# Kernel optimization log

Hardware: AMD Instinct MI355X
Metric: run time of the kernel (lower is better)

The kernel has to match this reference:

```python
import jax, jax.numpy as jnp
import numpy as np

D = 768          # wav2vec2-base hidden size
H = 4            # cross-attn heads
HD = D // H
B = 8
N = 1024         # w2v sequence length (target length)
T = 2000         # raw CQCC frames
N_GAT = 3
NUM_CLASSES = 2


def _p(key, shape, scale=0.02):
    return jax.random.normal(key, shape, dtype=jnp.float32) * scale


def layer_norm(x, g, b, eps=1e-5):
    m = x.mean(-1, keepdims=True)
    v = x.var(-1, keepdims=True)
    return (x - m) * jax.lax.rsqrt(v + eps) * g + b


def gelu(x):
    return jax.nn.gelu(x, approximate=False)


def conv1d(x, w, b):
    # x [B,C,T], w [O,I,K], padding=1 (same)
    y = jax.lax.conv_general_dilated(x, w, (1,), [(1, 1)], dimension_numbers=('NCH', 'OIH', 'NCH'))
    return y + b[None, :, None]


def batchnorm(x, g, b, m, v, eps=1e-5):
    # eval-mode BatchNorm1d on [B,C,T]
    return (x - m[None, :, None]) * jax.lax.rsqrt(v[None, :, None] + eps) * g[None, :, None] + b[None, :, None]


def interp_linear(x, target_len):
    # torch F.interpolate(mode='linear', align_corners=False); x [B,T,D] -> [B,target_len,D]
    t_in = x.shape[1]
    pos = (jnp.arange(target_len, dtype=jnp.float32) + 0.5) * (t_in / target_len) - 0.5
    pos = jnp.clip(pos, 0.0, t_in - 1.0)
    lo = jnp.floor(pos).astype(jnp.int32)
    hi = jnp.minimum(lo + 1, t_in - 1)
    w = (pos - lo.astype(jnp.float32))[None, :, None]
    return x[:, lo] * (1.0 - w) + x[:, hi] * w


def mha(q, k, v, in_w, in_b, out_w, out_b):
    # torch nn.MultiheadAttention, batch_first=True
    bb, nq, _ = q.shape
    nk = k.shape[1]
    wq, wk, wv = in_w[:D], in_w[D:2 * D], in_w[2 * D:]
    bq, bk, bv = in_b[:D], in_b[D:2 * D], in_b[2 * D:]
    qh = (q @ wq.T + bq).reshape(bb, nq, H, HD).transpose(0, 2, 1, 3)
    kh = (k @ wk.T + bk).reshape(bb, nk, H, HD).transpose(0, 2, 1, 3)
    vh = (v @ wv.T + bv).reshape(bb, nk, H, HD).transpose(0, 2, 1, 3)
    scores = jnp.einsum('bhqd,bhkd->bhqk', qh, kh) * (1.0 / np.sqrt(HD))
    alpha = jax.nn.softmax(scores, axis=-1)
    o = jnp.einsum('bhqk,bhkd->bhqd', alpha, vh).transpose(0, 2, 1, 3).reshape(bb, nq, D)
    return o @ out_w.T + out_b


def graph_attn(x, fc_w, fc_b, a_w, a_b):
    # GAT score on concat([h_i, h_j]) decomposes additively: e_ij = a_i.h_i + a_j.h_j + b
    h = x @ fc_w.T + fc_b                      # [B,N,D]
    s_i = h @ a_w[:D]                          # [B,N]
    s_j = h @ a_w[D:]                          # [B,N]
    e = s_i[:, :, None] + s_j[:, None, :] + a_b  # [B,N,N]
    alpha = jax.nn.softmax(e, axis=-1)
    return jnp.einsum('bij,bjd->bid', alpha, h)


def _forward(w2v, cqcc, conv1_w, conv1_b, bn1_g, bn1_b, bn1_m, bn1_v,
             conv2_w, conv2_b, bn2_g, bn2_b, bn2_m, bn2_v, pos_embed,
             lnq_g, lnq_b, lnkv_g, lnkv_b,
             a1_in_w, a1_in_b, a1_out_w, a1_out_b,
             a2_in_w, a2_in_b, a2_out_w, a2_out_b,
             gat_fc_w, gat_fc_b, gat_a_w, gat_a_b, gln_g, gln_b,
             clf_w1, clf_b1, clf_w2, clf_b2):
    # CQCC conv stack
    x = gelu(batchnorm(conv1d(cqcc, conv1_w, conv1_b), bn1_g, bn1_b, bn1_m, bn1_v))
    x = gelu(batchnorm(conv1d(x, conv2_w, conv2_b), bn2_g, bn2_b, bn2_m, bn2_v))  # [B,D,T]
    cq = interp_linear(x.transpose(0, 2, 1), w2v.shape[1])  # [B,N,D]
    # shared positional encoding
    n = w2v.shape[1]
    w = w2v + pos_embed[:, :n]
    cq = cq + pos_embed[:, :n]
    # bidirectional cross attention (norm_q / norm_kv shared across directions)
    out1 = mha(layer_norm(cq, lnq_g, lnq_b), layer_norm(w, lnkv_g, lnkv_b),
               layer_norm(w, lnkv_g, lnkv_b), a1_in_w, a1_in_b, a1_out_w, a1_out_b)
    out2 = mha(layer_norm(w, lnq_g, lnq_b), layer_norm(cq, lnkv_g, lnkv_b),
               layer_norm(cq, lnkv_g, lnkv_b), a2_in_w, a2_in_b, a2_out_w, a2_out_b)
    x = out1 + out2
    # 3 residual graph-attention blocks
    for l in range(N_GAT):
        res = x
        x = graph_attn(x, gat_fc_w[l], gat_fc_b[l], gat_a_w[l], gat_a_b[l])
        x = layer_norm(x + res, gln_g[l], gln_b[l])
    pooled = x.mean(axis=1)
    h = gelu(pooled @ clf_w1.T + clf_b1)
    return h @ clf_w2.T + clf_b2


def setup_inputs():
    ks = iter(jax.random.split(jax.random.key(0), 64))
    inp = {}
    inp['w2v'] = jax.random.normal(next(ks), (B, N, D), dtype=jnp.float32)
    inp['cqcc'] = jax.random.normal(next(ks), (B, 20, T), dtype=jnp.float32)
    inp['conv1_w'] = _p(next(ks), (128, 20, 3)); inp['conv1_b'] = jnp.zeros((128,), jnp.float32)
    inp['bn1_g'] = jnp.ones((128,), jnp.float32); inp['bn1_b'] = jnp.zeros((128,), jnp.float32)
    inp['bn1_m'] = jnp.zeros((128,), jnp.float32); inp['bn1_v'] = jnp.ones((128,), jnp.float32)
    inp['conv2_w'] = _p(next(ks), (D, 128, 3)); inp['conv2_b'] = jnp.zeros((D,), jnp.float32)
    inp['bn2_g'] = jnp.ones((D,), jnp.float32); inp['bn2_b'] = jnp.zeros((D,), jnp.float32)
    inp['bn2_m'] = jnp.zeros((D,), jnp.float32); inp['bn2_v'] = jnp.ones((D,), jnp.float32)
    inp['pos_embed'] = _p(next(ks), (1, 2000, D), 1.0)
    inp['lnq_g'] = jnp.ones((D,), jnp.float32); inp['lnq_b'] = jnp.zeros((D,), jnp.float32)
    inp['lnkv_g'] = jnp.ones((D,), jnp.float32); inp['lnkv_b'] = jnp.zeros((D,), jnp.float32)
    inp['a1_in_w'] = _p(next(ks), (3 * D, D)); inp['a1_in_b'] = jnp.zeros((3 * D,), jnp.float32)
    inp['a1_out_w'] = _p(next(ks), (D, D)); inp['a1_out_b'] = jnp.zeros((D,), jnp.float32)
    inp['a2_in_w'] = _p(next(ks), (3 * D, D)); inp['a2_in_b'] = jnp.zeros((3 * D,), jnp.float32)
    inp['a2_out_w'] = _p(next(ks), (D, D)); inp['a2_out_b'] = jnp.zeros((D,), jnp.float32)
    inp['gat_fc_w'] = _p(next(ks), (N_GAT, D, D)); inp['gat_fc_b'] = jnp.zeros((N_GAT, D), jnp.float32)
    inp['gat_a_w'] = _p(next(ks), (N_GAT, 2 * D)); inp['gat_a_b'] = jnp.zeros((N_GAT,), jnp.float32)
    inp['gln_g'] = jnp.ones((N_GAT, D), jnp.float32); inp['gln_b'] = jnp.zeros((N_GAT, D), jnp.float32)
    inp['clf_w1'] = _p(next(ks), (128, D)); inp['clf_b1'] = jnp.zeros((128,), jnp.float32)
    inp['clf_w2'] = _p(next(ks), (NUM_CLASSES, 128)); inp['clf_b2'] = jnp.zeros((NUM_CLASSES,), jnp.float32)
    return inp


def reference(w2v, cqcc, conv1_w, conv1_b, bn1_g, bn1_b, bn1_m, bn1_v,
              conv2_w, conv2_b, bn2_g, bn2_b, bn2_m, bn2_v, pos_embed,
              lnq_g, lnq_b, lnkv_g, lnkv_b,
              a1_in_w, a1_in_b, a1_out_w, a1_out_b,
              a2_in_w, a2_in_b, a2_out_w, a2_out_b,
              gat_fc_w, gat_fc_b, gat_a_w, gat_a_b, gln_g, gln_b,
              clf_w1, clf_b1, clf_w2, clf_b2):
    return _forward(w2v, cqcc, conv1_w, conv1_b, bn1_g, bn1_b, bn1_m, bn1_v,
                    conv2_w, conv2_b, bn2_g, bn2_b, bn2_m, bn2_v, pos_embed,
                    lnq_g, lnq_b, lnkv_g, lnkv_b,
                    a1_in_w, a1_in_b, a1_out_w, a1_out_b,
                    a2_in_w, a2_in_b, a2_out_w, a2_out_b,
                    gat_fc_w, gat_fc_b, gat_a_w, gat_a_b, gln_g, gln_b,
                    clf_w1, clf_b1, clf_w2, clf_b2)
```

## Files before the change

### kernel.cpp

```cpp
#include <hip/hip_runtime.h>
#include <math.h>

#define DD 768
#define NH 4
#define HDIM 192
#define BBATCH 8
#define NSEQ 1024
#define TLEN 2000
#define SLOT 6291456

typedef _Float16 h16;
typedef _Float16 half8v __attribute__((ext_vector_type(8)));
typedef _Float16 half4v __attribute__((ext_vector_type(4)));
typedef float f32x4 __attribute__((ext_vector_type(4)));

__device__ __forceinline__ float gelu_f(float x){
  return 0.5f * x * (1.0f + erff(x * 0.70710678118654752440f));
}
__device__ __forceinline__ float wave_sum(float v){
  #pragma unroll
  for (int off = 32; off; off >>= 1) v += __shfl_xor(v, off);
  return v;
}
__device__ __forceinline__ float wave_max(float v){
  #pragma unroll
  for (int off = 32; off; off >>= 1) v = fmaxf(v, __shfl_xor(v, off));
  return v;
}
__device__ __forceinline__ void gload16(const h16* g, h16* l){
  __builtin_amdgcn_global_load_lds(
      (const __attribute__((address_space(1))) void*)g,
      (__attribute__((address_space(3))) void*)l, 16, 0, 0);
}
__device__ __forceinline__ int xcd_remap(int orig, int nwg){
  int q = nwg >> 3, r = nwg & 7;
  int xcd = orig & 7, idx = orig >> 3;
  return (xcd < r ? xcd * (q + 1) : r * (q + 1) + (xcd - r) * q) + idx;
}

__global__ __launch_bounds__(256) void k_cast(const float* __restrict__ s,
    h16* __restrict__ d, int n){
  int i = blockIdx.x * 256 + threadIdx.x;
  if (i < n) d[i] = (h16)s[i];
}

__global__ __launch_bounds__(256) void k_conv1t(const float* __restrict__ cqcc,
    const float* __restrict__ w, const float* __restrict__ bias,
    const float* __restrict__ g, const float* __restrict__ be,
    const float* __restrict__ mm, const float* __restrict__ vv,
    float* __restrict__ out){
  __shared__ float xs[20][258];
  __shared__ float wsm[32*60];
  const int t0 = blockIdx.x * 256;
  const int ocg = blockIdx.y, b = blockIdx.z;
  const int tid = threadIdx.x;
  for (int idx = tid; idx < 20*258; idx += 256){
    int ic = idx / 258, tt = idx % 258;
    int t = t0 + tt - 1;
    xs[ic][tt] = (t >= 0 && t < TLEN) ? cqcc[((size_t)b*20 + ic)*TLEN + t] : 0.f;
  }
  for (int idx = tid; idx < 32*60; idx += 256)
    wsm[idx] = w[ocg*32*60 + idx];
  __syncthreads();
  int t = t0 + tid;
  if (t >= TLEN) return;
  float acc[32] = {};
  for (int ic = 0; ic < 20; ++ic){
    float x0 = xs[ic][tid], x1v = xs[ic][tid+1], x2v = xs[ic][tid+2];
    #pragma unroll
    for (int oc = 0; oc < 32; ++oc){
      const float* wp = &wsm[(oc*20 + ic)*3];
      acc[oc] += wp[0]*x0 + wp[1]*x1v + wp[2]*x2v;
    }
  }
  #pragma unroll 4
  for (int oc = 0; oc < 32; ++oc){
    int c = ocg*32 + oc;
    float s = rsqrtf(vv[c] + 1e-5f) * g[c];
    float val = (acc[oc] + bias[c] - mm[c]) * s + be[c];
    out[((size_t)b*128 + c)*TLEN + t] = gelu_f(val);
  }
}

__global__ __launch_bounds__(256) void k_im2col(const float* __restrict__ x1,
    h16* __restrict__ A2){
  int idx = blockIdx.x * 256 + threadIdx.x;
  if (idx >= 16000*384) return;
  int c = idx % 384, m = idx / 384;
  int b = m / TLEN, t = m % TLEN;
  int ic = c / 3, kh = c % 3;
  int ts = t + kh - 1;
  float v = (ts < 0 || ts >= TLEN) ? 0.f : x1[((size_t)b*128 + ic)*TLEN + ts];
  A2[idx] = (h16)v;
}

__global__ void k_bnprep(const float* __restrict__ cb, const float* __restrict__ g,
    const float* __restrict__ be, const float* __restrict__ m,
    const float* __restrict__ v, float* __restrict__ sc, float* __restrict__ off){
  int i = blockIdx.x * 256 + threadIdx.x;
  if (i >= DD) return;
  float s = g[i] * rsqrtf(v[i] + 1e-5f);
  sc[i] = s;
  off[i] = (cb[i] - m[i]) * s + be[i];
}

__global__ __launch_bounds__(256) void k_interp_ln(const h16* __restrict__ x2,
    const float* __restrict__ pe,
    const float* __restrict__ g1, const float* __restrict__ b1, h16* __restrict__ o1,
    const float* __restrict__ g2, const float* __restrict__ b2, h16* __restrict__ o2){
  __shared__ float ss[4], sqq[4];
  int row = blockIdx.x, tid = threadIdx.x;
  int b = row >> 10, i = row & 1023;
  float p = (i + 0.5f) * ((float)TLEN / (float)NSEQ) - 0.5f;
  p = fminf(fmaxf(p, 0.f), (float)(TLEN - 1));
  int lo = (int)floorf(p);
  int hi = min(lo + 1, TLEN - 1);
  float w = p - (float)lo;
  const h16* blo = x2 + ((size_t)b * TLEN + lo) * DD;
  const h16* bhi = x2 + ((size_t)b * TLEN + hi) * DD;
  const float* per = pe + (size_t)i * DD;
  float v[3]; float s = 0.f, sq = 0.f;
  #pragma unroll
  for (int j = 0; j < 3; ++j){
    int d = j * 256 + tid;
    float x = (float)blo[d] * (1.f - w) + (float)bhi[d] * w + per[d];
    v[j] = x; s += x; sq += x * x;
  }
  s = wave_sum(s); sq = wave_sum(sq);
  int wv = tid >> 6;
  if ((tid & 63) == 0){ ss[wv] = s; sqq[wv] = sq; }
  __syncthreads();
  s  = ss[0] + ss[1] + ss[2] + ss[3];
  sq = sqq[0] + sqq[1] + sqq[2] + sqq[3];
  float mean = s * (1.f / DD);
  float var  = sq * (1.f / DD) - mean * mean;
  float r = rsqrtf(var + 1e-5f);
  #pragma unroll
  for (int j = 0; j < 3; ++j){
    int d = j * 256 + tid;
    float xn = (v[j] - mean) * r;
    o1[(size_t)row * DD + d] = (h16)(xn * g1[d] + b1[d]);
    o2[(size_t)row * DD + d] = (h16)(xn * g2[d] + b2[d]);
  }
}

__global__ __launch_bounds__(256) void k_addpos_ln(const float* __restrict__ xin,
    const float* __restrict__ pe,
    const float* __restrict__ g1, const float* __restrict__ b1, h16* __restrict__ o1,
    const float* __restrict__ g2, const float* __restrict__ b2, h16* __restrict__ o2){
  __shared__ float ss[4], sqq[4];
  int row = blockIdx.x, tid = threadIdx.x;
  int i = row & 1023;
  const float* ip = xin + (size_t)row * DD;
  const float* per = pe + (size_t)i * DD;
  float v[3]; float s = 0.f, sq = 0.f;
  #pragma unroll
  for (int j = 0; j < 3; ++j){
    int d = j * 256 + tid;
    float x = ip[d] + per[d];
    v[j] = x; s += x; sq += x * x;
  }
  s = wave_sum(s); sq = wave_sum(sq);
  int wv = tid >> 6;
  if ((tid & 63) == 0){ ss[wv] = s; sqq[wv] = sq; }
  __syncthreads();
  s  = ss[0] + ss[1] + ss[2] + ss[3];
  sq = sqq[0] + sqq[1] + sqq[2] + sqq[3];
  float mean = s * (1.f / DD);
  float var  = sq * (1.f / DD) - mean * mean;
  float r = rsqrtf(var + 1e-5f);
  #pragma unroll
  for (int j = 0; j < 3; ++j){
    int d = j * 256 + tid;
    float xn = (v[j] - mean) * r;
    o1[(size_t)row * DD + d] = (h16)(xn * g1[d] + b1[d]);
    o2[(size_t)row * DD + d] = (h16)(xn * g2[d] + b2[d]);
  }
}

__global__ __launch_bounds__(256) void k_lnH(const h16* __restrict__ in,
    const float* __restrict__ ctx, const float* __restrict__ g,
    const float* __restrict__ be, h16* __restrict__ out){
  __shared__ float ss[4], sqq[4];
  int row = blockIdx.x, tid = threadIdx.x;
  const h16* ip = in + (size_t)row * DD;
  int b = row >> 10;
  float v[3]; float s = 0.f, sq = 0.f;
  #pragma unroll
  for (int j = 0; j < 3; ++j){
    int d = j * 256 + tid;
    float x = (float)ip[d] + ctx[b * DD + d];
    v[j] = x; s += x; sq += x * x;
  }
  s = wave_sum(s); sq = wave_sum(sq);
  int w = tid >> 6;
  if ((tid & 63) == 0){ ss[w] = s; sqq[w] = sq; }
  __syncthreads();
  s  = ss[0] + ss[1] + ss[2] + ss[3];
  sq = sqq[0] + sqq[1] + sqq[2] + sqq[3];
  float mean = s * (1.f / DD);
  float var  = sq * (1.f / DD) - mean * mean;
  float r = rsqrtf(var + 1e-5f);
  #pragma unroll
  for (int j = 0; j < 3; ++j){
    int d = j * 256 + tid;
    out[(size_t)row * DD + d] = (h16)((v[j] - mean) * r * g[d] + be[d]);
  }
}

#define GEMM_MAINLOOP(Abase, lda, Wbase, ldw, Kdim)                          \
  auto stage = [&](int buf, int kt){                                         \
    _Pragma("unroll")                                                        \
    for (int i = 0; i < 4; ++i){                                             \
      int p = i*256 + tid; int row = p >> 3; int ch = (p & 7) ^ (row & 7);   \
      gload16(Abase + (size_t)(m0+row)*lda + kt + ch*8, &Als[buf][p*8]);     \
    }                                                                        \
    _Pragma("unroll")                                                        \
    for (int i = 0; i < 4; ++i){                                             \
      int p = i*256 + tid; int row = p >> 3; int ch = (p & 7) ^ (row & 7);   \
      gload16(Wbase + (size_t)(n0+row)*ldw + kt + ch*8, &Bls[buf][p*8]);     \
    }                                                                        \
  };                                                                         \
  stage(0, 0);                                                               \
  const int nk = Kdim >> 6;                                                  \
  for (int t = 0; t < nk; ++t){                                              \
    const int cur = t & 1;                                                   \
    if (t + 1 < nk){                                                         \
      stage(cur ^ 1, (t + 1) << 6);                                          \
      asm volatile("s_waitcnt vmcnt(8)" ::: "memory");                       \
    } else {                                                                 \
      asm volatile("s_waitcnt vmcnt(0)" ::: "memory");                       \
    }                                                                        \
    __builtin_amdgcn_s_barrier();                                            \
    __builtin_amdgcn_sched_barrier(0);                                       \
    __builtin_amdgcn_s_setprio(1);                                           \
    _Pragma("unroll")                                                        \
    for (int kk = 0; kk < 2; ++kk){                                          \
      half8v af[4], bf[4];                                                   \
      _Pragma("unroll")                                                      \
      for (int mi = 0; mi < 4; ++mi){                                        \
        int row = wr*64 + mi*16 + lr;                                        \
        int chp = (kk*4 + lg) ^ (row & 7);                                   \
        af[mi] = *(const half8v*)&Als[cur][row*64 + chp*8];                  \
      }                                                                      \
      _Pragma("unroll")                                                      \
      for (int ni = 0; ni < 4; ++ni){                                        \
        int row = wc*64 + ni*16 + lr;                                        \
        int chp = (kk*4 + lg) ^ (row & 7);                                   \
        bf[ni] = *(const half8v*)&Bls[cur][row*64 + chp*8];                  \
      }                                                                      \
      _Pragma("unroll")                                                      \
      for (int mi = 0; mi < 4; ++mi)                                         \
        _Pragma("unroll")                                                    \
        for (int ni = 0; ni < 4; ++ni)                                       \
          acc[mi][ni] = __builtin_amdgcn_mfma_f32_16x16x32_f16(              \
              af[mi], bf[ni], acc[mi][ni], 0, 0, 0);                         \
    }                                                                        \
    __builtin_amdgcn_s_setprio(0);                                           \
    asm volatile("s_waitcnt lgkmcnt(0)" ::: "memory");                       \
    __builtin_amdgcn_sched_barrier(0);                                       \
    __builtin_amdgcn_s_barrier();                                            \
  }

__global__ __launch_bounds__(256) void k_gemm_h(
    const h16* __restrict__ A, const h16* __restrict__ W,
    int lda, int ldw, int ldc, int K,
    const float* __restrict__ bias, const float* __restrict__ sc,
    const float* __restrict__ off, const h16* __restrict__ addh,
    float* __restrict__ outf, h16* __restrict__ outh,
    const float* __restrict__ rdw, float* __restrict__ rdpart)
{
  __shared__ h16 Als[2][128*64];
  __shared__ h16 Bls[2][128*64];
  const int tid = threadIdx.x;
  const int gx = gridDim.x, gy = gridDim.y;
  const int wg = xcd_remap(blockIdx.x + gx * blockIdx.y, gx * gy);
  const int nidx = wg % gx;
  const int n0 = nidx * 128, m0 = (wg / gx) * 128;
  const int lane = tid & 63, wid = tid >> 6;
  const int wr = wid >> 1, wc = wid & 1;
  const int lr = lane & 15, lg = lane >> 4;
  f32x4 acc[4][4] = {};
  GEMM_MAINLOOP(A, lda, W, ldw, K)
  float rd[4][4] = {};
  #pragma unroll
  for (int mi = 0; mi < 4; ++mi){
    #pragma unroll
    for (int ni = 0; ni < 4; ++ni){
      int col = n0 + wc*64 + ni*16 + lr;
      int rowb = m0 + wr*64 + mi*16 + lg*4;
      float cb = bias ? bias[col] : 0.f;
      float aw = rdw ? rdw[col] : 0.f;
      #pragma unroll
      for (int r = 0; r < 4; ++r){
        size_t idx = (size_t)(rowb + r) * ldc + col;
        float v = acc[mi][ni][r];
        if (sc){ v = v * sc[col] + off[col]; v = gelu_f(v); }
        else v += cb;
        if (addh) v += (float)addh[idx];
        if (outf) outf[idx] = v;
        if (outh) outh[idx] = (h16)v;
        if (rdw) rd[mi][r] += v * aw;
      }
    }
  }
  if (rdw){
    #pragma unroll
    for (int mi = 0; mi < 4; ++mi){
      #pragma unroll
      for (int r = 0; r < 4; ++r){
        float p = rd[mi][r];
        #pragma unroll
        for (int o = 1; o < 16; o <<= 1) p += __shfl_xor(p, o);
        if (lr == 0){
          int row = m0 + wr*64 + mi*16 + lg*4 + r;
          rdpart[(size_t)row * 12 + nidx*2 + wc] = p;
        }
      }
    }
  }
}

__global__ __launch_bounds__(256) void k_gemm6(
    const h16* __restrict__ Lall, const h16* __restrict__ w6,
    const float* __restrict__ b1, const float* __restrict__ b2,
    h16* __restrict__ qkv6)
{
  __shared__ h16 Als[2][128*64];
  __shared__ h16 Bls[2][128*64];
  const int tid = threadIdx.x;
  const int gx = gridDim.x, gy = gridDim.y;
  const int nwg = gx * gy * 6;
  const int wg = xcd_remap(blockIdx.x + gx*(blockIdx.y + gy*blockIdx.z), nwg);
  const int n0 = (wg % gx) * 128;
  const int m0 = ((wg / gx) % gy) * 128;
  const int bz = wg / (gx * gy);
  const int aidx = (1468 >> (2*bz)) & 3;
  const h16* A = Lall + (size_t)aidx * SLOT;
  const h16* W = w6 + (size_t)bz * 589824;
  const float* bias = (bz < 3 ? b1 + bz*DD : b2 + (bz-3)*DD);
  h16* C = qkv6 + (size_t)bz * SLOT;
  const int lane = tid & 63, wid = tid >> 6;
  const int wr = wid >> 1, wc = wid & 1;
  const int lr = lane & 15, lg = lane >> 4;
  f32x4 acc[4][4] = {};
  GEMM_MAINLOOP(A, DD, W, DD, DD)
  #pragma unroll
  for (int mi = 0; mi < 4; ++mi){
    #pragma unroll
    for (int ni = 0; ni < 4; ++ni){
      int col = n0 + wc*64 + ni*16 + lr;
      int rowb = m0 + wr*64 + mi*16 + lg*4;
      float cb = bias[col];
      #pragma unroll
      for (int r = 0; r < 4; ++r)
        C[(size_t)(rowb + r) * DD + col] = (h16)(acc[mi][ni][r] + cb);
    }
  }
}

__global__ __launch_bounds__(256) void k_trV(const h16* __restrict__ Vh, int ldv,
    h16* __restrict__ VT){
  __shared__ h16 tile[64*64];
  const int z = blockIdx.z, b = z >> 2, h = z & 3;
  const int q0 = blockIdx.x * 64, d0 = blockIdx.y * 64;
  const int t = threadIdx.x;
  {
    int qq = t >> 2, ds = (t & 3) * 16;
    const h16* src = Vh + ((size_t)b*NSEQ + q0 + qq)*ldv + h*HDIM + d0 + ds;
    half8v v0 = *(const half8v*)src;
    half8v v1 = *(const half8v*)(src + 8);
    int c0 = (ds >> 3) ^ (qq & 7), c1 = ((ds >> 3) + 1) ^ (qq & 7);
    *(half8v*)&tile[qq*64 + c0*8] = v0;
    *(half8v*)&tile[qq*64 + c1*8] = v1;
  }
  __syncthreads();
  {
    int dd = t >> 2, qs = (t & 3) * 16;
    half8v o0, o1;
    #pragma unroll
    for (int j = 0; j < 8; ++j){
      int q = qs + j, q2 = qs + 8 + j;
      o0[j] = tile[q*64  + (((dd>>3) ^ (q&7))*8)  + (dd & 7)];
      o1[j] = tile[q2*64 + (((dd>>3) ^ (q2&7))*8) + (dd & 7)];
    }
    h16* dst = VT + (size_t)z*HDIM*NSEQ + (size_t)(d0+dd)*NSEQ + q0 + qs;
    *(half8v*)dst = o0;
    *(half8v*)(dst + 8) = o1;
  }
}

__global__ __launch_bounds__(256) void k_flash(const h16* __restrict__ Qp,
    const h16* __restrict__ Kp, const h16* __restrict__ VTp,
    h16* __restrict__ Op){
  __shared__ h16 Ks[2][32*192];
  __shared__ h16 Vs[2][192*32];
  __shared__ h16 Ps[4][16*32];
  const int tid = threadIdx.x;
  const int bh = blockIdx.x, qt = blockIdx.y;
  const int b = bh >> 2, h = bh & 3;
  const int q0 = qt * 64;
  const h16* Qg = Qp + (size_t)b*NSEQ*DD + h*HDIM;
  const h16* Kg = Kp + (size_t)b*NSEQ*DD + h*HDIM;
  const h16* Vg = VTp + (size_t)bh*HDIM*NSEQ;
  const int lane = tid & 63, wid = tid >> 6;
  const int lr = lane & 15, lg = lane >> 4;
  half8v qf[6];
  {
    int qrow = q0 + wid*16 + lr;
    #pragma unroll
    for (int ks = 0; ks < 6; ++ks)
      qf[ks] = *(const half8v*)(Qg + (size_t)qrow*DD + ks*32 + lg*8);
  }
  auto stageK = [&](int buf, int k0){
    #pragma unroll
    for (int i = 0; i < 3; ++i){
      int p = i*256 + tid;
      int row = p / 24, chp = p % 24;
      int ch = chp ^ (row & 7);
      gload16(Kg + (size_t)(k0+row)*DD + ch*8, &Ks[buf][p*8]);
    }
  };
  auto stageV = [&](int buf, int k0){
    #pragma unroll
    for (int i = 0; i < 3; ++i){
      int p = i*256 + tid;
      int row = p >> 2, chp = p & 3;
      int ch = chp ^ ((row >> 1) & 3);
      gload16(Vg + (size_t)row*NSEQ + k0 + ch*8, &Vs[buf][p*8]);
    }
  };
  stageK(0, 0); stageV(0, 0);
  f32x4 oacc[12] = {};
  float m_run[4] = {-1e30f, -1e30f, -1e30f, -1e30f};
  float l_run[4] = {};
  const float SC = 0.07216878364870322f;
  __syncthreads();
  for (int kt = 0; kt < 32; ++kt){
    const int cur = kt & 1;
    if (kt + 1 < 32){ stageK(cur^1, (kt+1)*32); stageV(cur^1, (kt+1)*32); }
    f32x4 sacc[2] = {};
    __builtin_amdgcn_s_setprio(1);
    #pragma unroll
    for (int ks = 0; ks < 6; ++ks){
      #pragma unroll
      for (int t = 0; t < 2; ++t){
        int krow = t*16 + lr;
        int ch = (ks*4 + lg) ^ (krow & 7);
        half8v kf = *(const half8v*)&Ks[cur][krow*192 + ch*8];
        sacc[t] = __builtin_amdgcn_mfma_f32_16x16x32_f16(qf[ks], kf, sacc[t], 0, 0, 0);
      }
    }
    __builtin_amdgcn_s_setprio(0);
    float mnew[4], c[4], psum[4];
    #pragma unroll
    for (int r = 0; r < 4; ++r){
      float mt = fmaxf(sacc[0][r], sacc[1][r]);
      #pragma unroll
      for (int off = 1; off < 16; off <<= 1) mt = fmaxf(mt, __shfl_xor(mt, off));
      mnew[r] = fmaxf(m_run[r], mt * SC);
      c[r] = __expf(m_run[r] - mnew[r]);
      psum[r] = 0.f;
    }
    #pragma unroll
    for (int t = 0; t < 2; ++t){
      #pragma unroll
      for (int r = 0; r < 4; ++r){
        float p = __expf(sacc[t][r] * SC - mnew[r]);
        psum[r] += p;
        int q = lg*4 + r, key = t*16 + lr;
        int ch = (t*2 + (lr>>3)) ^ ((q>>1) & 3);
        Ps[wid][q*32 + ch*8 + (key & 7)] = (h16)p;
      }
    }
    #pragma unroll
    for (int r = 0; r < 4; ++r){
      #pragma unroll
      for (int off = 1; off < 16; off <<= 1) psum[r] += __shfl_xor(psum[r], off);
      l_run[r] = l_run[r] * c[r] + psum[r];
      m_run[r] = mnew[r];
    }
    #pragma unroll
    for (int dt = 0; dt < 12; ++dt){
      f32x4 o = oacc[dt];
      o[0] *= c[0]; o[1] *= c[1]; o[2] *= c[2]; o[3] *= c[3];
      oacc[dt] = o;
    }
    asm volatile("s_waitcnt lgkmcnt(0)" ::: "memory");
    __builtin_amdgcn_sched_barrier(0);
    {
      int pch = lg ^ ((lr >> 1) & 3);
      half8v pf = *(const half8v*)&Ps[wid][lr*32 + pch*8];
      __builtin_amdgcn_s_setprio(1);
      #pragma unroll
      for (int dt = 0; dt < 12; ++dt){
        int drow = dt*16 + lr;
        int vch = lg ^ ((drow >> 1) & 3);
        half8v vf = *(const half8v*)&Vs[cur][drow*32 + vch*8];
        oacc[dt] = __builtin_amdgcn_mfma_f32_16x16x32_f16(pf, vf, oacc[dt], 0, 0, 0);
      }
      __builtin_amdgcn_s_setprio(0);
    }
    __syncthreads();
  }
  float inv[4];
  #pragma unroll
  for (int r = 0; r < 4; ++r) inv[r] = 1.0f / l_run[r];
  h16* Og = Op + (size_t)b*NSEQ*DD + h*HDIM;
  #pragma unroll
  for (int dt = 0; dt < 12; ++dt){
    #pragma unroll
    for (int r = 0; r < 4; ++r){
      int q = q0 + wid*16 + lg*4 + r;
      Og[(size_t)q*DD + dt*16 + lr] = (h16)(oacc[dt][r] * inv[r]);
    }
  }
}

__global__ __launch_bounds__(256) void k_softmax12(const float* __restrict__ part,
    float* __restrict__ y){
  __shared__ float red[4];
  int b = blockIdx.x, tid = threadIdx.x;
  float v[4]; float mx = -1e30f;
  #pragma unroll
  for (int j = 0; j < 4; ++j){
    int i = j * 256 + tid;
    const float* p = part + (size_t)(b * NSEQ + i) * 12;
    float s = 0.f;
    #pragma unroll
    for (int k = 0; k < 12; ++k) s += p[k];
    v[j] = s; mx = fmaxf(mx, s);
  }
  mx = wave_max(mx);
  if ((tid & 63) == 0) red[tid >> 6] = mx;
  __syncthreads();
  mx = fmaxf(fmaxf(red[0], red[1]), fmaxf(red[2], red[3]));
  __syncthreads();
  float s = 0.f;
  #pragma unroll
  for (int j = 0; j < 4; ++j){ v[j] = __expf(v[j] - mx); s += v[j]; }
  s = wave_sum(s);
  if ((tid & 63) == 0) red[tid >> 6] = s;
  __syncthreads();
  s = red[0] + red[1] + red[2] + red[3];
  float inv = 1.0f / s;
  #pragma unroll
  for (int j = 0; j < 4; ++j) y[b * NSEQ + j * 256 + tid] = v[j] * inv;
}

__global__ __launch_bounds__(256) void k_ctx1(const float* __restrict__ alpha,
    const h16* __restrict__ h, float* __restrict__ part){
  int d = blockIdx.x * 256 + threadIdx.x;
  int b = blockIdx.y, pc = blockIdx.z;
  if (d >= DD) return;
  float acc = 0.f;
  const h16* hp = h + ((size_t)b * NSEQ + pc * 64) * DD + d;
  const float* ap = alpha + b * NSEQ + pc * 64;
  #pragma unroll 4
  for (int j = 0; j < 64; ++j) acc += ap[j] * (float)hp[(size_t)j * DD];
  part[(size_t)(b * 16 + pc) * DD + d] = acc;
}
__global__ __launch_bounds__(256) void k_ctx2(const float* __restrict__ part,
    float scale, float* __restrict__ ctx){
  int d = blockIdx.x * 256 + threadIdx.x;
  int b = blockIdx.y;
  if (d >= DD) return;
  float acc = 0.f;
  #pragma unroll
  for (int p = 0; p < 16; ++p) acc += part[(size_t)(b * 16 + p) * DD + d];
  ctx[b * DD + d] = acc * scale;
}

__global__ __launch_bounds__(256) void k_pool1(const h16* __restrict__ x,
    float* __restrict__ part){
  int d = blockIdx.x * 256 + threadIdx.x;
  int b = blockIdx.y, pc = blockIdx.z;
  if (d >= DD) return;
  float acc = 0.f;
  const h16* xp = x + ((size_t)b * NSEQ + pc * 64) * DD + d;
  #pragma unroll 4
  for (int j = 0; j < 64; ++j) acc += (float)xp[(size_t)j * DD];
  part[(size_t)(b * 16 + pc) * DD + d] = acc;
}

__global__ __launch_bounds__(128) void k_clf(const float* __restrict__ pooled,
    const float* __restrict__ w1, const float* __restrict__ b1,
    const float* __restrict__ w2, const float* __restrict__ b2,
    float* __restrict__ out){
  __shared__ float pl[DD];
  __shared__ float h1[128];
  int b = blockIdx.x, tid = threadIdx.x;
  #pragma unroll
  for (int j = 0; j < 6; ++j) pl[j * 128 + tid] = pooled[b * DD + j * 128 + tid];
  __syncthreads();
  float acc = b1[tid];
  const float* wp = w1 + (size_t)tid * DD;
  for (int d = 0; d < DD; ++d) acc += pl[d] * wp[d];
  h1[tid] = gelu_f(acc);
  __syncthreads();
  if (tid < 2){
    float o = b2[tid];
    const float* w2p = w2 + tid * 128;
    for (int c = 0; c < 128; ++c) o += h1[c] * w2p[c];
    out[b * 2 + tid] = o;
  }
}

extern "C" void kernel_launch(void* const* d_in, const int* in_sizes, int n_in,
                              void* d_out, int out_size, void* d_ws, size_t ws_size,
                              hipStream_t stream){
  (void)in_sizes; (void)n_in; (void)out_size;
  const float* w2v      = (const float*)d_in[0];
  const float* cqcc     = (const float*)d_in[1];
  const float* conv1_w  = (const float*)d_in[2];
  const float* conv1_b  = (const float*)d_in[3];
  const float* bn1_g    = (const float*)d_in[4];
  const float* bn1_b    = (const float*)d_in[5];
  const float* bn1_m    = (const float*)d_in[6];
  const float* bn1_v    = (const float*)d_in[7];
  const float* conv2_w  = (const float*)d_in[8];
  const float* conv2_b  = (const float*)d_in[9];
  const float* bn2_g    = (const float*)d_in[10];
  const float* bn2_b    = (const float*)d_in[11];
  const float* bn2_m    = (const float*)d_in[12];
  const float* bn2_v    = (const float*)d_in[13];
  const float* pos_embed= (const float*)d_in[14];
  const float* lnq_g    = (const float*)d_in[15];
  const float* lnq_b    = (const float*)d_in[16];
  const float* lnkv_g   = (const float*)d_in[17];
  const float* lnkv_b   = (const float*)d_in[18];
  const float* a1_in_w  = (const float*)d_in[19];
  const float* a1_in_b  = (const float*)d_in[20];
  const float* a1_out_w = (const float*)d_in[21];
  const float* a1_out_b = (const float*)d_in[22];
  const float* a2_in_w  = (const float*)d_in[23];
  const float* a2_in_b  = (const float*)d_in[24];
  const float* a2_out_w = (const float*)d_in[25];
  const float* a2_out_b = (const float*)d_in[26];
  const float* gat_fc_w = (const float*)d_in[27];
  const float* gat_fc_b = (const float*)d_in[28];
  const float* gat_a_w  = (const float*)d_in[29];
  const float* gln_g    = (const float*)d_in[31];
  const float* gln_b    = (const float*)d_in[32];
  const float* clf_w1   = (const float*)d_in[33];
  const float* clf_b1   = (const float*)d_in[34];
  const float* clf_w2   = (const float*)d_in[35];
  const float* clf_b2   = (const float*)d_in[36];

  char* wsp = (char*)d_ws;
  auto F = [&](size_t bytes){ char* p = wsp; wsp += (bytes + 255) & ~(size_t)255; return p; };
  h16* xh      = (h16*)F(12582912);
  h16* Lall    = (h16*)F(4*12582912);
  h16* qkv6    = (h16*)F(6*12582912);
  h16* VT      = (h16*)F(12582912);
  h16* o1h     = (h16*)F(12582912);
  h16* w6      = (h16*)F(2*3538944);
  h16* w_a1out = (h16*)F(1179648);
  h16* w_a2out = (h16*)F(1179648);
  h16* w_gat   = (h16*)F(3538944);
  h16* w_c2    = (h16*)F(589824);
  float* scb   = (float*)F(3072);
  float* offb  = (float*)F(3072);
  float* alpha = (float*)F(32768);
  float* ctxb  = (float*)F(24576);
  float* pooled= (float*)F(24576);
  float* partb = (float*)F(393216);
  if ((size_t)(wsp - (char*)d_ws) > ws_size) return;

  float* x1  = (float*)Lall;
  h16*   A2  = Lall + 2*SLOT;
  h16*   x2h = qkv6;
  h16*   hh  = qkv6;

  const int NR = BBATCH * NSEQ;

  k_cast<<<(1769472+255)/256, 256, 0, stream>>>(a1_in_w,  w6,           1769472);
  k_cast<<<(1769472+255)/256, 256, 0, stream>>>(a2_in_w,  w6 + 1769472, 1769472);
  k_cast<<<(589824+255)/256,  256, 0, stream>>>(a1_out_w, w_a1out, 589824);
  k_cast<<<(589824+255)/256,  256, 0, stream>>>(a2_out_w, w_a2out, 589824);
  k_cast<<<(1769472+255)/256, 256, 0, stream>>>(gat_fc_w, w_gat,   1769472);
  k_cast<<<(294912+255)/256,  256, 0, stream>>>(conv2_w,  w_c2,    294912);
  k_bnprep<<<3, 256, 0, stream>>>(conv2_b, bn2_g, bn2_b, bn2_m, bn2_v, scb, offb);

  k_conv1t<<<dim3(8, 4, BBATCH), 256, 0, stream>>>(cqcc, conv1_w, conv1_b,
      bn1_g, bn1_b, bn1_m, bn1_v, x1);
  k_im2col<<<(16000*384+255)/256, 256, 0, stream>>>(x1, A2);
  k_gemm_h<<<dim3(6, 125), 256, 0, stream>>>(A2, w_c2, 384, 384, DD, 384,
      nullptr, scb, offb, nullptr, nullptr, x2h, nullptr, nullptr);

  k_interp_ln<<<NR, 256, 0, stream>>>(x2h, pos_embed,
      lnq_g, lnq_b, Lall, lnkv_g, lnkv_b, Lall + SLOT);
  k_addpos_ln<<<NR, 256, 0, stream>>>(w2v, pos_embed,
      lnq_g, lnq_b, Lall + 2*SLOT, lnkv_g, lnkv_b, Lall + 3*SLOT);

  k_gemm6<<<dim3(6, 64, 6), 256, 0, stream>>>(Lall, w6, a1_in_b, a2_in_b, qkv6);

  dim3 gflash(32, 16);

  k_trV<<<dim3(16, 3, 32), 256, 0, stream>>>(qkv6 + 2*(size_t)SLOT, DD, VT);
  k_flash<<<gflash, 256, 0, stream>>>(qkv6, qkv6 + (size_t)SLOT, VT, qkv6);
  k_gemm_h<<<dim3(6, 64), 256, 0, stream>>>(qkv6, w_a1out, DD, DD, DD, DD,
      a1_out_b, nullptr, nullptr, nullptr, nullptr, o1h, nullptr, nullptr);

  k_trV<<<dim3(16, 3, 32), 256, 0, stream>>>(qkv6 + 5*(size_t)SLOT, DD, VT);
  k_flash<<<gflash, 256, 0, stream>>>(qkv6 + 3*(size_t)SLOT, qkv6 + 4*(size_t)SLOT,
                                      VT, qkv6 + 3*(size_t)SLOT);
  k_gemm_h<<<dim3(6, 64), 256, 0, stream>>>(qkv6 + 3*(size_t)SLOT, w_a2out,
      DD, DD, DD, DD, a2_out_b, nullptr, nullptr, o1h, nullptr, xh, nullptr, nullptr);

  for (int l = 0; l < 3; ++l){
    k_gemm_h<<<dim3(6, 64), 256, 0, stream>>>(xh, w_gat + (size_t)l*589824,
        DD, DD, DD, DD, gat_fc_b + l*DD, nullptr, nullptr, nullptr,
        nullptr, hh, gat_a_w + l*2*DD + DD, partb);
    k_softmax12<<<BBATCH, 256, 0, stream>>>(partb, alpha);
    k_ctx1<<<dim3(3, BBATCH, 16), 256, 0, stream>>>(alpha, hh, partb);
    k_ctx2<<<dim3(3, BBATCH), 256, 0, stream>>>(partb, 1.0f, ctxb);
    k_lnH<<<NR, 256, 0, stream>>>(xh, ctxb, gln_g + l*DD, gln_b + l*DD, xh);
  }

  k_pool1<<<dim3(3, BBATCH, 16), 256, 0, stream>>>(xh, partb);
  k_ctx2<<<dim3(3, BBATCH), 256, 0, stream>>>(partb, 1.0f/NSEQ, pooled);
  k_clf<<<BBATCH, 128, 0, stream>>>(pooled, clf_w1, clf_b1, clf_w2, clf_b2,
                                    (float*)d_out);
}
```

Measured before the change: 623.0 us.

## Fuse im2col into conv2 GEMM via padded time-major fp16 layout and merge weight casts

conv1 now writes fp16 output in a zero-padded [B, T+2, 128] time-major layout. A new implicit-GEMM conv2 kernel reads the three shifted taps directly through a reordered weight matrix (kh-major), which removes the fp32 intermediate and the separate im2col pass. Five weight-cast launches are merged into one segmented kernel to cut launch overhead. The GEMM pads M to 2048 rows per batch, so some rows are computed and then discarded, and conv1's writes are now strided 64-byte chunks per thread.

```diff
diff --git a/kernel.cpp b/kernel.cpp
--- a/kernel.cpp
+++ b/kernel.cpp
@@ -8,6 +8,7 @@
 #define NSEQ 1024
 #define TLEN 2000
 #define SLOT 6291456
+#define XROW 256256
 
 typedef _Float16 h16;
 typedef _Float16 half8v __attribute__((ext_vector_type(8)));
@@ -38,17 +39,35 @@
   return (xcd < r ? xcd * (q + 1) : r * (q + 1) + (xcd - r) * q) + idx;
 }
 
-__global__ __launch_bounds__(256) void k_cast(const float* __restrict__ s,
-    h16* __restrict__ d, int n){
+struct CastArgs {
+  const float* s[5];
+  h16* d[5];
+  int cum[6];
+};
+__global__ __launch_bounds__(256) void k_cast5(CastArgs a, int total){
   int i = blockIdx.x * 256 + threadIdx.x;
-  if (i < n) d[i] = (h16)s[i];
+  if (i >= total) return;
+  int seg = 0;
+  #pragma unroll
+  for (int t = 1; t < 5; ++t) seg += (i >= a.cum[t]);
+  int off = i - a.cum[seg];
+  a.d[seg][off] = (h16)a.s[seg][off];
+}
+
+__global__ __launch_bounds__(256) void k_castc2(const float* __restrict__ s,
+    h16* __restrict__ d){
+  int i = blockIdx.x * 256 + threadIdx.x;
+  if (i >= 294912) return;
+  int oc = i / 384, rem = i % 384;
+  int ic = rem / 3, kh = rem % 3;
+  d[oc * 384 + kh * 128 + ic] = (h16)s[i];
 }
 
 __global__ __launch_bounds__(256) void k_conv1t(const float* __restrict__ cqcc,
     const float* __restrict__ w, const float* __restrict__ bias,
     const float* __restrict__ g, const float* __restrict__ be,
     const float* __restrict__ mm, const float* __restrict__ vv,
-    float* __restrict__ out){
+    h16* __restrict__ X){
   __shared__ float xs[20][258];
   __shared__ float wsm[32*60];
   const int t0 = blockIdx.x * 256;
@@ -73,25 +92,24 @@
       acc[oc] += wp[0]*x0 + wp[1]*x1v + wp[2]*x2v;
     }
   }
+  h16* dst = X + (size_t)b*XROW + (size_t)(t+1)*128 + ocg*32;
   #pragma unroll 4
   for (int oc = 0; oc < 32; ++oc){
     int c = ocg*32 + oc;
     float s = rsqrtf(vv[c] + 1e-5f) * g[c];
     float val = (acc[oc] + bias[c] - mm[c]) * s + be[c];
-    out[((size_t)b*128 + c)*TLEN + t] = gelu_f(val);
-  }
-}
-
-__global__ __launch_bounds__(256) void k_im2col(const float* __restrict__ x1,
-    h16* __restrict__ A2){
-  int idx = blockIdx.x * 256 + threadIdx.x;
-  if (idx >= 16000*384) return;
-  int c = idx % 384, m = idx / 384;
-  int b = m / TLEN, t = m % TLEN;
-  int ic = c / 3, kh = c % 3;
-  int ts = t + kh - 1;
-  float v = (ts < 0 || ts >= TLEN) ? 0.f : x1[((size_t)b*128 + ic)*TLEN + ts];
-  A2[idx] = (h16)v;
+    dst[oc] = (h16)gelu_f(val);
+  }
+  if (t == 0){
+    h16* z = X + (size_t)b*XROW + ocg*32;
+    #pragma unroll
+    for (int oc = 0; oc < 32; ++oc) z[oc] = (h16)0.f;
+  }
+  if (t == TLEN-1){
+    h16* z = X + (size_t)b*XROW + (size_t)2001*128 + ocg*32;
+    #pragma unroll
+    for (int oc = 0; oc < 32; ++oc) z[oc] = (h16)0.f;
+  }
 }
 
 __global__ void k_bnprep(const float* __restrict__ cb, const float* __restrict__ g,
@@ -321,6 +339,92 @@
   }
 }
 
+__global__ __launch_bounds__(256) void k_conv2g(
+    const h16* __restrict__ X, const h16* __restrict__ W,
+    const float* __restrict__ sc, const float* __restrict__ off,
+    h16* __restrict__ out)
+{
+  __shared__ h16 Als[2][128*64];
+  __shared__ h16 Bls[2][128*64];
+  const int tid = threadIdx.x;
+  const int gx = gridDim.x, gy = gridDim.y;
+  const int wg = xcd_remap(blockIdx.x + gx * blockIdx.y, gx * gy);
+  const int n0 = (wg % gx) * 128, m0 = (wg / gx) * 128;
+  const int lane = tid & 63, wid = tid >> 6;
+  const int wr = wid >> 1, wc = wid & 1;
+  const int lr = lane & 15, lg = lane >> 4;
+  f32x4 acc[4][4] = {};
+  auto stage = [&](int buf, int kt){
+    #pragma unroll
+    for (int i = 0; i < 4; ++i){
+      int p = i*256 + tid; int row = p >> 3; int ch = (p & 7) ^ (row & 7);
+      int rm = m0 + row, b = rm >> 11, t = rm & 2047;
+      gload16(X + (size_t)b*XROW + (size_t)t*128 + kt + ch*8, &Als[buf][p*8]);
+    }
+    #pragma unroll
+    for (int i = 0; i < 4; ++i){
+      int p = i*256 + tid; int row = p >> 3; int ch = (p & 7) ^ (row & 7);
+      gload16(W + (size_t)(n0+row)*384 + kt + ch*8, &Bls[buf][p*8]);
+    }
+  };
+  stage(0, 0);
+  const int nk = 6;
+  for (int t = 0; t < nk; ++t){
+    const int cur = t & 1;
+    if (t + 1 < nk){
+      stage(cur ^ 1, (t + 1) << 6);
+      asm volatile("s_waitcnt vmcnt(8)" ::: "memory");
+    } else {
+      asm volatile("s_waitcnt vmcnt(0)" ::: "memory");
+    }
+    __builtin_amdgcn_s_barrier();
+    __builtin_amdgcn_sched_barrier(0);
+    __builtin_amdgcn_s_setprio(1);
+    #pragma unroll
+    for (int kk = 0; kk < 2; ++kk){
+      half8v af[4], bf[4];
+      #pragma unroll
+      for (int mi = 0; mi < 4; ++mi){
+        int row = wr*64 + mi*16 + lr;
+        int chp = (kk*4 + lg) ^ (row & 7);
+        af[mi] = *(const half8v*)&Als[cur][row*64 + chp*8];
+      }
+      #pragma unroll
+      for (int ni = 0; ni < 4; ++ni){
+        int row = wc*64 + ni*16 + lr;
+        int chp = (kk*4 + lg) ^ (row & 7);
+        bf[ni] = *(const half8v*)&Bls[cur][row*64 + chp*8];
+      }
+      #pragma unroll
+      for (int mi = 0; mi < 4; ++mi)
+        #pragma unroll
+        for (int ni = 0; ni < 4; ++ni)
+          acc[mi][ni] = __builtin_amdgcn_mfma_f32_16x16x32_f16(
+              af[mi], bf[ni], acc[mi][ni], 0, 0, 0);
+    }
+    __builtin_amdgcn_s_setprio(0);
+    asm volatile("s_waitcnt lgkmcnt(0)" ::: "memory");
+    __builtin_amdgcn_sched_barrier(0);
+    __builtin_amdgcn_s_barrier();
+  }
+  #pragma unroll
+  for (int mi = 0; mi < 4; ++mi){
+    #pragma unroll
+    for (int ni = 0; ni < 4; ++ni){
+      int col = n0 + wc*64 + ni*16 + lr;
+      int rowb = m0 + wr*64 + mi*16 + lg*4;
+      #pragma unroll
+      for (int r = 0; r < 4; ++r){
+        int rm = rowb + r, b = rm >> 11, t = rm & 2047;
+        if (t < TLEN){
+          float v = acc[mi][ni][r] * sc[col] + off[col];
+          out[((size_t)b*TLEN + t)*DD + col] = (h16)gelu_f(v);
+        }
+      }
+    }
+  }
+}
+
 __global__ __launch_bounds__(256) void k_gemm6(
     const h16* __restrict__ Lall, const h16* __restrict__ w6,
     const float* __restrict__ b1, const float* __restrict__ b2,
@@ -667,26 +771,30 @@
   float* partb = (float*)F(393216);
   if ((size_t)(wsp - (char*)d_ws) > ws_size) return;
 
-  float* x1  = (float*)Lall;
-  h16*   A2  = Lall + 2*SLOT;
-  h16*   x2h = qkv6;
-  h16*   hh  = qkv6;
+  h16* X   = Lall;
+  h16* x2h = qkv6;
+  h16* hh  = qkv6;
 
   const int NR = BBATCH * NSEQ;
 
-  k_cast<<<(1769472+255)/256, 256, 0, stream>>>(a1_in_w,  w6,           1769472);
-  k_cast<<<(1769472+255)/256, 256, 0, stream>>>(a2_in_w,  w6 + 1769472, 1769472);
-  k_cast<<<(589824+255)/256,  256, 0, stream>>>(a1_out_w, w_a1out, 589824);
-  k_cast<<<(589824+255)/256,  256, 0, stream>>>(a2_out_w, w_a2out, 589824);
-  k_cast<<<(1769472+255)/256, 256, 0, stream>>>(gat_fc_w, w_gat,   1769472);
-  k_cast<<<(294912+255)/256,  256, 0, stream>>>(conv2_w,  w_c2,    294912);
+  {
+    CastArgs ca;
+    ca.s[0]=a1_in_w;  ca.d[0]=w6;            int n0=1769472;
+    ca.s[1]=a2_in_w;  ca.d[1]=w6+1769472;    int n1=1769472;
+    ca.s[2]=a1_out_w; ca.d[2]=w_a1out;       int n2=589824;
+    ca.s[3]=a2_out_w; ca.d[3]=w_a2out;       int n3=589824;
+    ca.s[4]=gat_fc_w; ca.d[4]=w_gat;         int n4=1769472;
+    ca.cum[0]=0; ca.cum[1]=n0; ca.cum[2]=n0+n1; ca.cum[3]=n0+n1+n2;
+    ca.cum[4]=n0+n1+n2+n3; ca.cum[5]=n0+n1+n2+n3+n4;
+    int total = ca.cum[5];
+    k_cast5<<<(total+255)/256, 256, 0, stream>>>(ca, total);
+  }
+  k_castc2<<<(294912+255)/256, 256, 0, stream>>>(conv2_w, w_c2);
   k_bnprep<<<3, 256, 0, stream>>>(conv2_b, bn2_g, bn2_b, bn2_m, bn2_v, scb, offb);
 
   k_conv1t<<<dim3(8, 4, BBATCH), 256, 0, stream>>>(cqcc, conv1_w, conv1_b,
-      bn1_g, bn1_b, bn1_m, bn1_v, x1);
-  k_im2col<<<(16000*384+255)/256, 256, 0, stream>>>(x1, A2);
-  k_gemm_h<<<dim3(6, 125), 256, 0, stream>>>(A2, w_c2, 384, 384, DD, 384,
-      nullptr, scb, offb, nullptr, nullptr, x2h, nullptr, nullptr);
+      bn1_g, bn1_b, bn1_m, bn1_v, X);
+  k_conv2g<<<dim3(6, 128), 256, 0, stream>>>(X, w_c2, scb, offb, x2h);
 
   k_interp_ln<<<NR, 256, 0, stream>>>(x2h, pos_embed,
       lnq_g, lnq_b, Lall, lnkv_g, lnkv_b, Lall + SLOT);
```

Result: no change. 631.6 us (+1.4%).
